# Kernel tuning notes

Hardware: AMD Instinct MI355X
Metric: run time of the kernel (lower is better)

## Reference

```python
import jax, jax.numpy as jnp
import numpy as np

D = 64       # memory_dim
STEPS = 2


def setup_inputs() -> dict:
    key = jax.random.key(0)
    ks = jax.random.split(key, 20)
    N, M, R = 4096, 256, 512
    s = 0.05
    return {
        "coords": jax.random.normal(ks[0], (N, 3), jnp.float32) * 3.0,
        "memory_slots": jax.random.normal(ks[1], (M, D), jnp.float32),
        "anchor_keys": jax.random.normal(ks[2], (M, D), jnp.float32),
        "residue_positions": jax.random.normal(ks[3], (R, 3), jnp.float32) * 3.0,
        "residue_radii": jax.random.uniform(ks[4], (R,), jnp.float32, 0.5, 2.0),
        "W1": jax.random.normal(ks[5], (3, D), jnp.float32) * s,
        "b1": jnp.zeros((D,), jnp.float32),
        "W2": jax.random.normal(ks[6], (D, D), jnp.float32) * s,
        "b2": jnp.zeros((D,), jnp.float32),
        "Wg1": jax.random.normal(ks[7], (2 * D + 2, D), jnp.float32) * s,
        "bg1": jnp.zeros((D,), jnp.float32),
        "Wg2": jax.random.normal(ks[8], (D, 1), jnp.float32) * s,
        "bg2": jnp.zeros((1,), jnp.float32),
        "Wu1": jax.random.normal(ks[9], (2 * D + 2, D), jnp.float32) * s,
        "bu1": jnp.zeros((D,), jnp.float32),
        "Wu2": jax.random.normal(ks[10], (D, D), jnp.float32) * s,
        "bu2": jnp.zeros((D,), jnp.float32),
    }


def _step(points, qe, mem, keys, rpos, rrad,
          Wg1, bg1, Wg2, bg2, Wu1, bu1, Wu2, bu2):
    N = qe.shape[0]
    M = mem.shape[0]
    # attention read
    logits = (qe @ keys.T) / jnp.sqrt(jnp.asarray(D, qe.dtype))     # [N, M]
    rw = jax.nn.softmax(logits, axis=-1)                             # [N, M]
    mc = rw @ mem                                                    # [N, D]
    # SDF gate: cdist(points, residue_positions) -> min over residues
    sq = jnp.sum((points[:, None, :] - rpos[None, :, :]) ** 2, axis=-1)
    geo = jnp.sqrt(jnp.maximum(sq, 0.0))                             # [N, R]
    sdf = jnp.min(geo - rrad[None, :], axis=-1, keepdims=True)       # [N, 1]
    sg = jax.nn.sigmoid(4.0 * sdf)                                   # [N, 1]
    # broadcast-concat -> [N, M, 2D+2]
    write_in = jnp.concatenate([
        jnp.broadcast_to(mc[:, None, :], (N, M, D)),
        jnp.broadcast_to(mem[None, :, :], (N, M, D)),
        rw[:, :, None],
        jnp.broadcast_to(sg[:, None, :], (N, M, 1)),
    ], axis=-1)
    gate = jax.nn.sigmoid(jax.nn.silu(write_in @ Wg1 + bg1) @ Wg2 + bg2)
    gate = jnp.mean(gate, axis=0)                                    # [M, 1]
    delta = jax.nn.silu(write_in @ Wu1 + bu1) @ Wu2 + bu2
    delta = jnp.mean(delta, axis=0)                                  # [M, D]
    mem2 = mem + gate * delta
    return mc, rw, gate, sg, mem2


def reference(coords, memory_slots, anchor_keys, residue_positions, residue_radii,
              W1, b1, W2, b2, Wg1, bg1, Wg2, bg2, Wu1, bu1, Wu2, bu2):
    points = coords.reshape(-1, 3)
    qe = jax.nn.silu(points @ W1 + b1) @ W2 + b2                     # coord_proj
    mem = memory_slots
    for _ in range(max(STEPS, 1)):
        mc, rw, gate, sg, mem = _step(points, qe, mem, anchor_keys,
                                      residue_positions, residue_radii,
                                      Wg1, bg1, Wg2, bg2, Wu1, bu1, Wu2, bu2)
        qe = qe + 0.5 * mc
    # (memory_context, read_weights, write_gate, symbolic_gate, updated_memory)
    return mc, rw, gate[:, 0], sg[:, 0], mem
```

## Files before the change

### kernel.cpp

```cpp
#include <hip/hip_runtime.h>
#include <hip/hip_bf16.h>
#include <math.h>

#define DD 64
#define LOG2E 1.44269504f
#define LN2 0.69314718f
#define NEG_L2E (-1.44269504f)

__device__ __forceinline__ float frcp(float x) { return __builtin_amdgcn_rcpf(x); }
__device__ __forceinline__ float fsig(float x) { return frcp(1.0f + __expf(-x)); }
__device__ __forceinline__ float fsilu(float x) { return x * fsig(x); }
__device__ __forceinline__ float rcp1p(float e) {
  float y = 1.0f + e;
  float r = __uint_as_float(0x7EF127EAu - __float_as_uint(y));
  return r * fmaf(-y, r, 2.0f);
}

__global__ __launch_bounds__(DD) void k_coord(
    const float* __restrict__ coords, const float* __restrict__ W1,
    const float* __restrict__ b1, const float* __restrict__ W2,
    const float* __restrict__ b2, float* __restrict__ qe, int N) {
  int n = blockIdx.x;
  int k = threadIdx.x;
  __shared__ float h[DD];
  float px = coords[n * 3 + 0], py = coords[n * 3 + 1], pz = coords[n * 3 + 2];
  float t = px * W1[k] + py * W1[DD + k] + pz * W1[2 * DD + k] + b1[k];
  h[k] = fsilu(t);
  __syncthreads();
  float q = b2[k];
#pragma unroll 8
  for (int j = 0; j < DD; j++) q += h[j] * W2[j * DD + k];
  qe[n * DD + k] = q;
}

__global__ __launch_bounds__(256) void k_prep(
    const float* __restrict__ keys, float* __restrict__ keysT, int M) {
  int j = blockIdx.x;
  int t = threadIdx.x;
  keysT[j * M + t] = keys[t * DD + j];
}

__global__ __launch_bounds__(DD) void k_scale(
    const float* __restrict__ Wg1, const float* __restrict__ Wu1,
    const float* __restrict__ Wg2, float* __restrict__ wg1r_n,
    float* __restrict__ wu1r_n, float* __restrict__ w2n) {
  int k = threadIdx.x;
  wg1r_n[k] = Wg1[128 * DD + k] * NEG_L2E;
  wu1r_n[k] = Wu1[128 * DD + k] * NEG_L2E;
  w2n[k] = -Wg2[k] * LN2;
}

__global__ __launch_bounds__(256) void k_sdf(
    const float* __restrict__ rpos, const float* __restrict__ rrad,
    const float* __restrict__ coords, float* __restrict__ sg_out, int N, int R) {
  int wv = threadIdx.x >> 6, ln = threadIdx.x & 63;
  int n = blockIdx.x * 4 + wv;
  if (n >= N) return;
  float px = coords[n * 3], py = coords[n * 3 + 1], pz = coords[n * 3 + 2];
  float mn = 1e30f;
  for (int r = ln; r < R; r += 64) {
    float dx = px - rpos[r * 3], dy = py - rpos[r * 3 + 1], dz = pz - rpos[r * 3 + 2];
    float d = sqrtf(dx * dx + dy * dy + dz * dz) - rrad[r];
    mn = fminf(mn, d);
  }
  mn = fminf(mn, __shfl_xor(mn, 32, 64));
  mn = fminf(mn, __shfl_xor(mn, 16, 64));
  mn = fminf(mn, __shfl_xor(mn, 8, 64));
  mn = fminf(mn, __shfl_xor(mn, 4, 64));
  mn = fminf(mn, __shfl_xor(mn, 2, 64));
  mn = fminf(mn, __shfl_xor(mn, 1, 64));
  if (ln == 0) sg_out[n] = fsig(4.0f * mn);
}

__global__ __launch_bounds__(256) void k_attn(
    const float* __restrict__ qe_in, const float* __restrict__ keysT,
    const float* __restrict__ mem, const float* __restrict__ sg,
    const float* __restrict__ Wg1, const float* __restrict__ bg1,
    const float* __restrict__ Wu1, const float* __restrict__ bu1,
    float* __restrict__ rw_out, float* __restrict__ rwT,
    float* __restrict__ mc_out, float* __restrict__ qe_io,
    float* __restrict__ AgT4, float* __restrict__ Au, int N, int M, int NCH2) {
  int bx = blockIdx.x;
  int c = bx % NCH2;
  int j2 = bx / NCH2;
  int n0 = c * 128 + j2 * 4;
  int t = threadIdx.x;
  int wv = t >> 6, ln = t & 63;
  __shared__ __align__(16) float rws[4][256];
  __shared__ __align__(16) float mcs[4][DD];
  __shared__ float red[4][4], red2[4][4];
  __shared__ float part[4][4][DD];
  float lg[4] = {0.f, 0.f, 0.f, 0.f};
#pragma unroll 8
  for (int j = 0; j < DD; j++) {
    float kv = keysT[j * M + t];
    lg[0] += qe_in[(size_t)(n0 + 0) * DD + j] * kv;
    lg[1] += qe_in[(size_t)(n0 + 1) * DD + j] * kv;
    lg[2] += qe_in[(size_t)(n0 + 2) * DD + j] * kv;
    lg[3] += qe_in[(size_t)(n0 + 3) * DD + j] * kv;
  }
  float e[4];
#pragma unroll
  for (int q = 0; q < 4; q++) {
    float x = lg[q] * 0.125f;
    lg[q] = x;
    float mx = x;
    mx = fmaxf(mx, __shfl_xor(mx, 32, 64));
    mx = fmaxf(mx, __shfl_xor(mx, 16, 64));
    mx = fmaxf(mx, __shfl_xor(mx, 8, 64));
    mx = fmaxf(mx, __shfl_xor(mx, 4, 64));
    mx = fmaxf(mx, __shfl_xor(mx, 2, 64));
    mx = fmaxf(mx, __shfl_xor(mx, 1, 64));
    if (ln == 0) red[q][wv] = mx;
  }
  __syncthreads();
#pragma unroll
  for (int q = 0; q < 4; q++) {
    float mx = fmaxf(fmaxf(red[q][0], red[q][1]), fmaxf(red[q][2], red[q][3]));
    float ee = __expf(lg[q] - mx);
    e[q] = ee;
    float sm = ee;
    sm += __shfl_xor(sm, 32, 64);
    sm += __shfl_xor(sm, 16, 64);
    sm += __shfl_xor(sm, 8, 64);
    sm += __shfl_xor(sm, 4, 64);
    sm += __shfl_xor(sm, 2, 64);
    sm += __shfl_xor(sm, 1, 64);
    if (ln == 0) red2[q][wv] = sm;
  }
  __syncthreads();
  float rv4[4];
#pragma unroll
  for (int q = 0; q < 4; q++) {
    float tot = red2[q][0] + red2[q][1] + red2[q][2] + red2[q][3];
    float rv = e[q] * frcp(tot);
    rw_out[(size_t)(n0 + q) * M + t] = rv;
    rws[q][t] = rv;
    rv4[q] = rv;
  }
  *reinterpret_cast<float4*>(&rwT[(size_t)t * N + n0]) =
      make_float4(rv4[0], rv4[1], rv4[2], rv4[3]);
  __syncthreads();
  float acc[4] = {0.f, 0.f, 0.f, 0.f};
#pragma unroll
  for (int mm4 = 0; mm4 < 16; mm4++) {
    int mbase = wv * 64 + mm4 * 4;
    const float4 r0 = *reinterpret_cast<const float4*>(&rws[0][mbase]);
    const float4 r1 = *reinterpret_cast<const float4*>(&rws[1][mbase]);
    const float4 r2 = *reinterpret_cast<const float4*>(&rws[2][mbase]);
    const float4 r3 = *reinterpret_cast<const float4*>(&rws[3][mbase]);
    float m0v = mem[(size_t)(mbase + 0) * DD + ln];
    float m1v = mem[(size_t)(mbase + 1) * DD + ln];
    float m2v = mem[(size_t)(mbase + 2) * DD + ln];
    float m3v = mem[(size_t)(mbase + 3) * DD + ln];
    acc[0] += r0.x * m0v + r0.y * m1v + r0.z * m2v + r0.w * m3v;
    acc[1] += r1.x * m0v + r1.y * m1v + r1.z * m2v + r1.w * m3v;
    acc[2] += r2.x * m0v + r2.y * m1v + r2.z * m2v + r2.w * m3v;
    acc[3] += r3.x * m0v + r3.y * m1v + r3.z * m2v + r3.w * m3v;
  }
#pragma unroll
  for (int q = 0; q < 4; q++) part[q][wv][ln] = acc[q];
  __syncthreads();
  {
    int q = wv;
    float mc = part[q][0][ln] + part[q][1][ln] + part[q][2][ln] + part[q][3][ln];
    mc_out[(size_t)(n0 + q) * DD + ln] = mc;
    qe_io[(size_t)(n0 + q) * DD + ln] =
        qe_in[(size_t)(n0 + q) * DD + ln] + 0.5f * mc;
    mcs[q][ln] = mc;
  }
  __syncthreads();
  {
    const float* W = (wv < 2) ? Wg1 : Wu1;
    const float* bb = (wv < 2) ? bg1 : bu1;
    int qa = (wv & 1) * 2, qb = qa + 1;
    int k = ln;
    float w129 = W[129 * DD + k];
    float bbk = bb[k];
    float a0 = bbk + sg[n0 + qa] * w129;
    float a1 = bbk + sg[n0 + qb] * w129;
#pragma unroll
    for (int j4 = 0; j4 < 16; j4++) {
      const float4 ma = *reinterpret_cast<const float4*>(&mcs[qa][j4 * 4]);
      const float4 mb = *reinterpret_cast<const float4*>(&mcs[qb][j4 * 4]);
      float w0 = W[(size_t)(j4 * 4 + 0) * DD + k];
      float w1 = W[(size_t)(j4 * 4 + 1) * DD + k];
      float w2v = W[(size_t)(j4 * 4 + 2) * DD + k];
      float w3 = W[(size_t)(j4 * 4 + 3) * DD + k];
      a0 += ma.x * w0 + ma.y * w1 + ma.z * w2v + ma.w * w3;
      a1 += mb.x * w0 + mb.y * w1 + mb.z * w2v + mb.w * w3;
    }
    a0 *= NEG_L2E;
    a1 *= NEG_L2E;
    if (wv < 2) {
      AgT4[((size_t)(k >> 2) * N + n0 + qa) * 4 + (k & 3)] = a0;
      AgT4[((size_t)(k >> 2) * N + n0 + qb) * 4 + (k & 3)] = a1;
    } else {
      Au[(size_t)(n0 + qa) * DD + k] = a0;
      Au[(size_t)(n0 + qb) * DD + k] = a1;
    }
  }
}

__global__ __launch_bounds__(128) void k_b(
    const float* __restrict__ mem, const float* __restrict__ Wg1,
    const float* __restrict__ Wu1, float* __restrict__ BgT,
    float* __restrict__ Bu, int M) {
  int m = blockIdx.x;
  int t = threadIdx.x;
  __shared__ float row[DD];
  if (t < DD) row[t] = mem[m * DD + t];
  __syncthreads();
  int k = t & 63;
  const float* W = (t < DD) ? Wg1 : Wu1;
  float b = 0.f;
#pragma unroll 8
  for (int j = 0; j < DD; j++) b += row[j] * W[(DD + j) * DD + k];
  b *= NEG_L2E;
  if (t < DD) BgT[k * M + m] = b;
  else Bu[m * DD + k] = b;
}

__global__ __launch_bounds__(128) void k_write(
    const float* __restrict__ rwT, const float* __restrict__ AgT4,
    const float* __restrict__ Au, const float* __restrict__ BgT,
    const float* __restrict__ Bu, const float* __restrict__ wg1r_n,
    const float* __restrict__ wu1r_n, const float* __restrict__ w2n,
    const float* __restrict__ bg2, float* __restrict__ gate_part,
    float* __restrict__ su_part, int N, int M, int NCH2) {
  int bx = blockIdx.x;
  int c = bx % NCH2;
  int m0 = (bx / NCH2) * 4;
  int wave = threadIdx.x >> 6, lane = threadIdx.x & 63;
  int n0 = __builtin_amdgcn_readfirstlane(c * 128 + wave * 64);

  float rwl[4];
#pragma unroll
  for (int mi = 0; mi < 4; mi++)
    rwl[mi] = rwT[(size_t)(m0 + mi) * N + n0 + lane];
  float gacc[4] = {0.f, 0.f, 0.f, 0.f};
  const float* agp = &AgT4[(size_t)(n0 + lane) * 4];
  float4 ag_cur = *reinterpret_cast<const float4*>(agp);
#pragma unroll
  for (int k4 = 0; k4 < 16; k4++) {
    float4 ag_next = (k4 < 15)
        ? *reinterpret_cast<const float4*>(agp + (size_t)(k4 + 1) * N * 4)
        : ag_cur;
    float agv[4] = {ag_cur.x, ag_cur.y, ag_cur.z, ag_cur.w};
#pragma unroll
    for (int kk = 0; kk < 4; kk++) {
      int k = k4 * 4 + kk;
      const float4 bg4 =
          *reinterpret_cast<const float4*>(&BgT[k * M + m0]);
      float bgv[4] = {bg4.x, bg4.y, bg4.z, bg4.w};
      float wr = wg1r_n[k];
      float w2 = w2n[k];
#pragma unroll
      for (int mi = 0; mi < 4; mi++) {
        float tp = fmaf(rwl[mi], wr, agv[kk] + bgv[mi]);
        float ee = __builtin_amdgcn_exp2f(tp);
        gacc[mi] = fmaf(tp * w2, rcp1p(ee), gacc[mi]);
      }
    }
    ag_cur = ag_next;
  }
  float bg2v = bg2[0];
  float gate[4];
#pragma unroll
  for (int mi = 0; mi < 4; mi++) {
    float g = fsig(gacc[mi] + bg2v);
    g += __shfl_xor(g, 32, 64);
    g += __shfl_xor(g, 16, 64);
    g += __shfl_xor(g, 8, 64);
    g += __shfl_xor(g, 4, 64);
    g += __shfl_xor(g, 2, 64);
    g += __shfl_xor(g, 1, 64);
    gate[mi] = g;
  }

  float bu[4];
#pragma unroll
  for (int mi = 0; mi < 4; mi++) bu[mi] = Bu[(size_t)(m0 + mi) * DD + lane];
  float wu = wu1r_n[lane];
  float su[4] = {0.f, 0.f, 0.f, 0.f};
  const float* Aup = Au + (size_t)n0 * DD + lane;
  const float* r0p = rwT + (size_t)(m0 + 0) * N + n0;
  const float* r1p = rwT + (size_t)(m0 + 1) * N + n0;
  const float* r2p = rwT + (size_t)(m0 + 2) * N + n0;
  const float* r3p = rwT + (size_t)(m0 + 3) * N + n0;
  float au_cur = Aup[0];
#pragma unroll 8
  for (int i = 0; i < 64; i++) {
    float au_next = (i < 63) ? Aup[(size_t)(i + 1) * DD] : au_cur;
    float rvs[4] = {r0p[i], r1p[i], r2p[i], r3p[i]};
#pragma unroll
    for (int mi = 0; mi < 4; mi++) {
      float tp = fmaf(rvs[mi], wu, au_cur + bu[mi]);
      float ee = __builtin_amdgcn_exp2f(tp);
      su[mi] = fmaf(tp, rcp1p(ee), su[mi]);
    }
    au_cur = au_next;
  }

  __shared__ float su_s[2][4][DD];
  __shared__ float g_s[2][4];
#pragma unroll
  for (int mi = 0; mi < 4; mi++) su_s[wave][mi][lane] = su[mi];
  if (lane == 0) {
#pragma unroll
    for (int mi = 0; mi < 4; mi++) g_s[wave][mi] = gate[mi];
  }
  __syncthreads();
  if (threadIdx.x < DD) {
    int k = threadIdx.x;
#pragma unroll
    for (int mi = 0; mi < 4; mi++) {
      su_part[((size_t)(m0 + mi) * NCH2 + c) * DD + k] =
          (su_s[0][mi][k] + su_s[1][mi][k]) * (-LN2);
      if (k == 0)
        gate_part[(m0 + mi) * NCH2 + c] = g_s[0][mi] + g_s[1][mi];
    }
  }
}

__global__ __launch_bounds__(128) void k_reduce_b(
    const float* __restrict__ gate_part, const float* __restrict__ su_part,
    const float* __restrict__ Wu2, const float* __restrict__ bu2,
    const float* __restrict__ mem_in, const float* __restrict__ Wg1,
    const float* __restrict__ Wu1, float* __restrict__ mem_out,
    float* __restrict__ gate_out, float* __restrict__ BgT,
    float* __restrict__ Bu, int N, int M, int NCH2) {
  int m = blockIdx.x;
  int t = threadIdx.x;
  int k = t & 63;
  __shared__ float su_s[DD];
  __shared__ float row[DD];
  __shared__ float gmean;
  float invN = frcp((float)N);
  if (t < DD) {
    float s = 0.f;
    for (int c = 0; c < NCH2; c++) s += su_part[((size_t)m * NCH2 + c) * DD + k];
    su_s[k] = s * invN;
    if (k == 0) {
      float g = 0.f;
      for (int c = 0; c < NCH2; c++) g += gate_part[m * NCH2 + c];
      gmean = g * invN;
    }
  }
  __syncthreads();
  if (t < DD) {
    float delta = bu2[k];
#pragma unroll 8
    for (int j = 0; j < DD; j++) delta += su_s[j] * Wu2[j * DD + k];
    float v = mem_in[m * DD + k] + gmean * delta;
    mem_out[m * DD + k] = v;
    row[k] = v;
    if (k == 0) gate_out[m] = gmean;
  }
  __syncthreads();
  const float* W = (t < DD) ? Wg1 : Wu1;
  float b = 0.f;
#pragma unroll 8
  for (int j = 0; j < DD; j++) b += row[j] * W[(DD + j) * DD + k];
  b *= NEG_L2E;
  if (t < DD) BgT[k * M + m] = b;
  else Bu[m * DD + k] = b;
}

extern "C" void kernel_launch(void* const* d_in, const int* in_sizes, int n_in,
                              void* d_out, int out_size, void* d_ws, size_t ws_size,
                              hipStream_t stream) {
  const float* coords = (const float*)d_in[0];
  const float* memory_slots = (const float*)d_in[1];
  const float* anchor_keys = (const float*)d_in[2];
  const float* rpos = (const float*)d_in[3];
  const float* rrad = (const float*)d_in[4];
  const float* W1 = (const float*)d_in[5];
  const float* b1 = (const float*)d_in[6];
  const float* W2 = (const float*)d_in[7];
  const float* b2 = (const float*)d_in[8];
  const float* Wg1 = (const float*)d_in[9];
  const float* bg1 = (const float*)d_in[10];
  const float* Wg2 = (const float*)d_in[11];
  const float* bg2 = (const float*)d_in[12];
  const float* Wu1 = (const float*)d_in[13];
  const float* bu1 = (const float*)d_in[14];
  const float* Wu2 = (const float*)d_in[15];
  const float* bu2 = (const float*)d_in[16];

  const int N = in_sizes[0] / 3;
  const int M = in_sizes[1] / DD;
  const int R = in_sizes[4];
  const int NCH2 = N / 128;

  float* out = (float*)d_out;
  float* out_mc = out;
  float* out_rw = out_mc + (size_t)N * DD;
  float* out_gate = out_rw + (size_t)N * M;
  float* out_sg = out_gate + M;
  float* out_mem = out_sg + N;

  float* ws = (float*)d_ws;
  float* qe = ws;        ws += (size_t)N * DD;
  float* AgT4 = ws;      ws += (size_t)N * DD;
  float* Au = ws;        ws += (size_t)N * DD;
  float* rwT = ws;       ws += (size_t)M * N;
  float* keysT = ws;     ws += (size_t)DD * M;
  float* BgT = ws;       ws += (size_t)DD * M;
  float* Bu = ws;        ws += (size_t)M * DD;
  float* wg1r_n = ws;    ws += DD;
  float* wu1r_n = ws;    ws += DD;
  float* w2n = ws;       ws += DD;
  float* gate_part = ws; ws += (size_t)M * NCH2;
  float* su_part = ws;   ws += (size_t)M * NCH2 * DD;

  k_coord<<<N, DD, 0, stream>>>(coords, W1, b1, W2, b2, qe, N);
  k_prep<<<DD, M, 0, stream>>>(anchor_keys, keysT, M);
  k_scale<<<1, DD, 0, stream>>>(Wg1, Wu1, Wg2, wg1r_n, wu1r_n, w2n);
  k_sdf<<<N / 4, 256, 0, stream>>>(rpos, rrad, coords, out_sg, N, R);
  k_b<<<M, 128, 0, stream>>>(memory_slots, Wg1, Wu1, BgT, Bu, M);

  const float* mem_cur = memory_slots;
  for (int step = 0; step < 2; step++) {
    k_attn<<<N / 4, 256, 0, stream>>>(qe, keysT, mem_cur, out_sg, Wg1, bg1, Wu1,
                                      bu1, out_rw, rwT, out_mc, qe, AgT4, Au,
                                      N, M, NCH2);
    k_write<<<(M / 4) * NCH2, 128, 0, stream>>>(rwT, AgT4, Au, BgT, Bu,
                                                wg1r_n, wu1r_n, w2n, bg2,
                                                gate_part, su_part, N, M, NCH2);
    k_reduce_b<<<M, 128, 0, stream>>>(gate_part, su_part, Wu2, bu2, mem_cur,
                                      Wg1, Wu1, out_mem, out_gate, BgT, Bu,
                                      N, M, NCH2);
    mem_cur = out_mem;
  }
}
```

Baseline: 144.3 us.

## Fuse setup kernels into one launch and split write kernel into gate/update blocks

Merges the five setup kernels (coord projection, key transpose, weight scaling, SDF gate, B precompute) into one block-indexed k_setup launch to cut launch overhead. It also splits k_write over a second grid dimension so the gate and update reductions run in separate blocks in parallel instead of serially in one block. This doubles k_write's block count and shortens each block's critical path, at the cost of reading rwT twice and running some setup blocks with idle threads.

```diff
diff --git a/kernel.cpp b/kernel.cpp
--- a/kernel.cpp
+++ b/kernel.cpp
@@ -16,60 +16,77 @@
   return r * fmaf(-y, r, 2.0f);
 }
 
-__global__ __launch_bounds__(DD) void k_coord(
+__global__ __launch_bounds__(256) void k_setup(
     const float* __restrict__ coords, const float* __restrict__ W1,
     const float* __restrict__ b1, const float* __restrict__ W2,
-    const float* __restrict__ b2, float* __restrict__ qe, int N) {
-  int n = blockIdx.x;
-  int k = threadIdx.x;
-  __shared__ float h[DD];
-  float px = coords[n * 3 + 0], py = coords[n * 3 + 1], pz = coords[n * 3 + 2];
-  float t = px * W1[k] + py * W1[DD + k] + pz * W1[2 * DD + k] + b1[k];
-  h[k] = fsilu(t);
-  __syncthreads();
-  float q = b2[k];
-#pragma unroll 8
-  for (int j = 0; j < DD; j++) q += h[j] * W2[j * DD + k];
-  qe[n * DD + k] = q;
-}
-
-__global__ __launch_bounds__(256) void k_prep(
-    const float* __restrict__ keys, float* __restrict__ keysT, int M) {
-  int j = blockIdx.x;
-  int t = threadIdx.x;
-  keysT[j * M + t] = keys[t * DD + j];
-}
-
-__global__ __launch_bounds__(DD) void k_scale(
-    const float* __restrict__ Wg1, const float* __restrict__ Wu1,
-    const float* __restrict__ Wg2, float* __restrict__ wg1r_n,
-    float* __restrict__ wu1r_n, float* __restrict__ w2n) {
-  int k = threadIdx.x;
-  wg1r_n[k] = Wg1[128 * DD + k] * NEG_L2E;
-  wu1r_n[k] = Wu1[128 * DD + k] * NEG_L2E;
-  w2n[k] = -Wg2[k] * LN2;
-}
-
-__global__ __launch_bounds__(256) void k_sdf(
+    const float* __restrict__ b2, const float* __restrict__ keys,
     const float* __restrict__ rpos, const float* __restrict__ rrad,
-    const float* __restrict__ coords, float* __restrict__ sg_out, int N, int R) {
-  int wv = threadIdx.x >> 6, ln = threadIdx.x & 63;
-  int n = blockIdx.x * 4 + wv;
-  if (n >= N) return;
-  float px = coords[n * 3], py = coords[n * 3 + 1], pz = coords[n * 3 + 2];
-  float mn = 1e30f;
-  for (int r = ln; r < R; r += 64) {
-    float dx = px - rpos[r * 3], dy = py - rpos[r * 3 + 1], dz = pz - rpos[r * 3 + 2];
-    float d = sqrtf(dx * dx + dy * dy + dz * dz) - rrad[r];
-    mn = fminf(mn, d);
-  }
-  mn = fminf(mn, __shfl_xor(mn, 32, 64));
-  mn = fminf(mn, __shfl_xor(mn, 16, 64));
-  mn = fminf(mn, __shfl_xor(mn, 8, 64));
-  mn = fminf(mn, __shfl_xor(mn, 4, 64));
-  mn = fminf(mn, __shfl_xor(mn, 2, 64));
-  mn = fminf(mn, __shfl_xor(mn, 1, 64));
-  if (ln == 0) sg_out[n] = fsig(4.0f * mn);
+    const float* __restrict__ mem, const float* __restrict__ Wg1,
+    const float* __restrict__ Wu1, const float* __restrict__ Wg2,
+    float* __restrict__ qe, float* __restrict__ keysT,
+    float* __restrict__ sg_out, float* __restrict__ BgT,
+    float* __restrict__ Bu, float* __restrict__ wg1r_n,
+    float* __restrict__ wu1r_n, float* __restrict__ w2n, int N, int M, int R) {
+  int bx = blockIdx.x;
+  int NB4 = N / 4;
+  if (bx < NB4) {
+    int sub = threadIdx.x >> 6, k = threadIdx.x & 63;
+    int n = bx * 4 + sub;
+    __shared__ float h[4][DD];
+    float px = coords[n * 3 + 0], py = coords[n * 3 + 1], pz = coords[n * 3 + 2];
+    float t = px * W1[k] + py * W1[DD + k] + pz * W1[2 * DD + k] + b1[k];
+    h[sub][k] = fsilu(t);
+    __syncthreads();
+    float q = b2[k];
+#pragma unroll 8
+    for (int j = 0; j < DD; j++) q += h[sub][j] * W2[j * DD + k];
+    qe[(size_t)n * DD + k] = q;
+  } else if (bx < 2 * NB4) {
+    int wv = threadIdx.x >> 6, ln = threadIdx.x & 63;
+    int n = (bx - NB4) * 4 + wv;
+    float px = coords[n * 3], py = coords[n * 3 + 1], pz = coords[n * 3 + 2];
+    float mn = 1e30f;
+    for (int r = ln; r < R; r += 64) {
+      float dx = px - rpos[r * 3], dy = py - rpos[r * 3 + 1],
+            dz = pz - rpos[r * 3 + 2];
+      float d = sqrtf(dx * dx + dy * dy + dz * dz) - rrad[r];
+      mn = fminf(mn, d);
+    }
+    mn = fminf(mn, __shfl_xor(mn, 32, 64));
+    mn = fminf(mn, __shfl_xor(mn, 16, 64));
+    mn = fminf(mn, __shfl_xor(mn, 8, 64));
+    mn = fminf(mn, __shfl_xor(mn, 4, 64));
+    mn = fminf(mn, __shfl_xor(mn, 2, 64));
+    mn = fminf(mn, __shfl_xor(mn, 1, 64));
+    if (ln == 0) sg_out[n] = fsig(4.0f * mn);
+  } else if (bx < 2 * NB4 + DD) {
+    int j = bx - 2 * NB4;
+    int t = threadIdx.x;
+    keysT[j * M + t] = keys[t * DD + j];
+  } else if (bx < 2 * NB4 + DD + M) {
+    int m = bx - (2 * NB4 + DD);
+    int t = threadIdx.x;
+    __shared__ float row[DD];
+    if (t < DD) row[t] = mem[m * DD + t];
+    __syncthreads();
+    if (t < 128) {
+      int k = t & 63;
+      const float* W = (t < DD) ? Wg1 : Wu1;
+      float b = 0.f;
+#pragma unroll 8
+      for (int j = 0; j < DD; j++) b += row[j] * W[(DD + j) * DD + k];
+      b *= NEG_L2E;
+      if (t < DD) BgT[k * M + m] = b;
+      else Bu[m * DD + k] = b;
+    }
+  } else {
+    int k = threadIdx.x;
+    if (k < DD) {
+      wg1r_n[k] = Wg1[128 * DD + k] * NEG_L2E;
+      wu1r_n[k] = Wu1[128 * DD + k] * NEG_L2E;
+      w2n[k] = -Wg2[k] * LN2;
+    }
+  }
 }
 
 __global__ __launch_bounds__(256) void k_attn(
@@ -202,25 +219,6 @@
   }
 }
 
-__global__ __launch_bounds__(128) void k_b(
-    const float* __restrict__ mem, const float* __restrict__ Wg1,
-    const float* __restrict__ Wu1, float* __restrict__ BgT,
-    float* __restrict__ Bu, int M) {
-  int m = blockIdx.x;
-  int t = threadIdx.x;
-  __shared__ float row[DD];
-  if (t < DD) row[t] = mem[m * DD + t];
-  __syncthreads();
-  int k = t & 63;
-  const float* W = (t < DD) ? Wg1 : Wu1;
-  float b = 0.f;
-#pragma unroll 8
-  for (int j = 0; j < DD; j++) b += row[j] * W[(DD + j) * DD + k];
-  b *= NEG_L2E;
-  if (t < DD) BgT[k * M + m] = b;
-  else Bu[m * DD + k] = b;
-}
-
 __global__ __launch_bounds__(128) void k_write(
     const float* __restrict__ rwT, const float* __restrict__ AgT4,
     const float* __restrict__ Au, const float* __restrict__ BgT,
@@ -234,91 +232,90 @@
   int wave = threadIdx.x >> 6, lane = threadIdx.x & 63;
   int n0 = __builtin_amdgcn_readfirstlane(c * 128 + wave * 64);
 
-  float rwl[4];
-#pragma unroll
-  for (int mi = 0; mi < 4; mi++)
-    rwl[mi] = rwT[(size_t)(m0 + mi) * N + n0 + lane];
-  float gacc[4] = {0.f, 0.f, 0.f, 0.f};
-  const float* agp = &AgT4[(size_t)(n0 + lane) * 4];
-  float4 ag_cur = *reinterpret_cast<const float4*>(agp);
-#pragma unroll
-  for (int k4 = 0; k4 < 16; k4++) {
-    float4 ag_next = (k4 < 15)
-        ? *reinterpret_cast<const float4*>(agp + (size_t)(k4 + 1) * N * 4)
-        : ag_cur;
-    float agv[4] = {ag_cur.x, ag_cur.y, ag_cur.z, ag_cur.w};
-#pragma unroll
-    for (int kk = 0; kk < 4; kk++) {
-      int k = k4 * 4 + kk;
-      const float4 bg4 =
-          *reinterpret_cast<const float4*>(&BgT[k * M + m0]);
-      float bgv[4] = {bg4.x, bg4.y, bg4.z, bg4.w};
-      float wr = wg1r_n[k];
-      float w2 = w2n[k];
+  if (blockIdx.y == 0) {
+    __shared__ float g_s[2][4];
+    float rwl[4];
+#pragma unroll
+    for (int mi = 0; mi < 4; mi++)
+      rwl[mi] = rwT[(size_t)(m0 + mi) * N + n0 + lane];
+    float gacc[4] = {0.f, 0.f, 0.f, 0.f};
+    const float* agp = &AgT4[(size_t)(n0 + lane) * 4];
+    float4 ag_cur = *reinterpret_cast<const float4*>(agp);
+#pragma unroll
+    for (int k4 = 0; k4 < 16; k4++) {
+      float4 ag_next = (k4 < 15)
+          ? *reinterpret_cast<const float4*>(agp + (size_t)(k4 + 1) * N * 4)
+          : ag_cur;
+      float agv[4] = {ag_cur.x, ag_cur.y, ag_cur.z, ag_cur.w};
+#pragma unroll
+      for (int kk = 0; kk < 4; kk++) {
+        int k = k4 * 4 + kk;
+        const float4 bg4 =
+            *reinterpret_cast<const float4*>(&BgT[k * M + m0]);
+        float bgv[4] = {bg4.x, bg4.y, bg4.z, bg4.w};
+        float wr = wg1r_n[k];
+        float w2 = w2n[k];
+#pragma unroll
+        for (int mi = 0; mi < 4; mi++) {
+          float tp = fmaf(rwl[mi], wr, agv[kk] + bgv[mi]);
+          float ee = __builtin_amdgcn_exp2f(tp);
+          gacc[mi] = fmaf(tp * w2, rcp1p(ee), gacc[mi]);
+        }
+      }
+      ag_cur = ag_next;
+    }
+    float bg2v = bg2[0];
+#pragma unroll
+    for (int mi = 0; mi < 4; mi++) {
+      float g = fsig(gacc[mi] + bg2v);
+      g += __shfl_xor(g, 32, 64);
+      g += __shfl_xor(g, 16, 64);
+      g += __shfl_xor(g, 8, 64);
+      g += __shfl_xor(g, 4, 64);
+      g += __shfl_xor(g, 2, 64);
+      g += __shfl_xor(g, 1, 64);
+      if (lane == 0) g_s[wave][mi] = g;
+    }
+    __syncthreads();
+    if (threadIdx.x < 4) {
+      int mi = threadIdx.x;
+      gate_part[(m0 + mi) * NCH2 + c] = g_s[0][mi] + g_s[1][mi];
+    }
+  } else {
+    __shared__ float su_s[2][4][DD];
+    float bu[4];
+#pragma unroll
+    for (int mi = 0; mi < 4; mi++) bu[mi] = Bu[(size_t)(m0 + mi) * DD + lane];
+    float wu = wu1r_n[lane];
+    float su[4] = {0.f, 0.f, 0.f, 0.f};
+    const float* Aup = Au + (size_t)n0 * DD + lane;
+    const float* r0p = rwT + (size_t)(m0 + 0) * N + n0;
+    const float* r1p = rwT + (size_t)(m0 + 1) * N + n0;
+    const float* r2p = rwT + (size_t)(m0 + 2) * N + n0;
+    const float* r3p = rwT + (size_t)(m0 + 3) * N + n0;
+    float au_cur = Aup[0];
+#pragma unroll 8
+    for (int i = 0; i < 64; i++) {
+      float au_next = (i < 63) ? Aup[(size_t)(i + 1) * DD] : au_cur;
+      float rvs[4] = {r0p[i], r1p[i], r2p[i], r3p[i]};
 #pragma unroll
       for (int mi = 0; mi < 4; mi++) {
-        float tp = fmaf(rwl[mi], wr, agv[kk] + bgv[mi]);
+        float tp = fmaf(rvs[mi], wu, au_cur + bu[mi]);
         float ee = __builtin_amdgcn_exp2f(tp);
-        gacc[mi] = fmaf(tp * w2, rcp1p(ee), gacc[mi]);
+        su[mi] = fmaf(tp, rcp1p(ee), su[mi]);
       }
-    }
-    ag_cur = ag_next;
-  }
-  float bg2v = bg2[0];
-  float gate[4];
-#pragma unroll
-  for (int mi = 0; mi < 4; mi++) {
-    float g = fsig(gacc[mi] + bg2v);
-    g += __shfl_xor(g, 32, 64);
-    g += __shfl_xor(g, 16, 64);
-    g += __shfl_xor(g, 8, 64);
-    g += __shfl_xor(g, 4, 64);
-    g += __shfl_xor(g, 2, 64);
-    g += __shfl_xor(g, 1, 64);
-    gate[mi] = g;
-  }
-
-  float bu[4];
-#pragma unroll
-  for (int mi = 0; mi < 4; mi++) bu[mi] = Bu[(size_t)(m0 + mi) * DD + lane];
-  float wu = wu1r_n[lane];
-  float su[4] = {0.f, 0.f, 0.f, 0.f};
-  const float* Aup = Au + (size_t)n0 * DD + lane;
-  const float* r0p = rwT + (size_t)(m0 + 0) * N + n0;
-  const float* r1p = rwT + (size_t)(m0 + 1) * N + n0;
-  const float* r2p = rwT + (size_t)(m0 + 2) * N + n0;
-  const float* r3p = rwT + (size_t)(m0 + 3) * N + n0;
-  float au_cur = Aup[0];
-#pragma unroll 8
-  for (int i = 0; i < 64; i++) {
-    float au_next = (i < 63) ? Aup[(size_t)(i + 1) * DD] : au_cur;
-    float rvs[4] = {r0p[i], r1p[i], r2p[i], r3p[i]};
-#pragma unroll
-    for (int mi = 0; mi < 4; mi++) {
-      float tp = fmaf(rvs[mi], wu, au_cur + bu[mi]);
-      float ee = __builtin_amdgcn_exp2f(tp);
-      su[mi] = fmaf(tp, rcp1p(ee), su[mi]);
-    }
-    au_cur = au_next;
-  }
-
-  __shared__ float su_s[2][4][DD];
-  __shared__ float g_s[2][4];
-#pragma unroll
-  for (int mi = 0; mi < 4; mi++) su_s[wave][mi][lane] = su[mi];
-  if (lane == 0) {
-#pragma unroll
-    for (int mi = 0; mi < 4; mi++) g_s[wave][mi] = gate[mi];
-  }
-  __syncthreads();
-  if (threadIdx.x < DD) {
-    int k = threadIdx.x;
-#pragma unroll
-    for (int mi = 0; mi < 4; mi++) {
-      su_part[((size_t)(m0 + mi) * NCH2 + c) * DD + k] =
-          (su_s[0][mi][k] + su_s[1][mi][k]) * (-LN2);
-      if (k == 0)
-        gate_part[(m0 + mi) * NCH2 + c] = g_s[0][mi] + g_s[1][mi];
+      au_cur = au_next;
+    }
+#pragma unroll
+    for (int mi = 0; mi < 4; mi++) su_s[wave][mi][lane] = su[mi];
+    __syncthreads();
+    if (threadIdx.x < DD) {
+      int k = threadIdx.x;
+#pragma unroll
+      for (int mi = 0; mi < 4; mi++) {
+        su_part[((size_t)(m0 + mi) * NCH2 + c) * DD + k] =
+            (su_s[0][mi][k] + su_s[1][mi][k]) * (-LN2);
+      }
     }
   }
 }
@@ -414,20 +411,19 @@
   float* gate_part = ws; ws += (size_t)M * NCH2;
   float* su_part = ws;   ws += (size_t)M * NCH2 * DD;
 
-  k_coord<<<N, DD, 0, stream>>>(coords, W1, b1, W2, b2, qe, N);
-  k_prep<<<DD, M, 0, stream>>>(anchor_keys, keysT, M);
-  k_scale<<<1, DD, 0, stream>>>(Wg1, Wu1, Wg2, wg1r_n, wu1r_n, w2n);
-  k_sdf<<<N / 4, 256, 0, stream>>>(rpos, rrad, coords, out_sg, N, R);
-  k_b<<<M, 128, 0, stream>>>(memory_slots, Wg1, Wu1, BgT, Bu, M);
+  int setup_blocks = (N / 4) * 2 + DD + M + 1;
+  k_setup<<<setup_blocks, 256, 0, stream>>>(
+      coords, W1, b1, W2, b2, anchor_keys, rpos, rrad, memory_slots, Wg1, Wu1,
+      Wg2, qe, keysT, out_sg, BgT, Bu, wg1r_n, wu1r_n, w2n, N, M, R);
 
   const float* mem_cur = memory_slots;
   for (int step = 0; step < 2; step++) {
     k_attn<<<N / 4, 256, 0, stream>>>(qe, keysT, mem_cur, out_sg, Wg1, bg1, Wu1,
                                       bu1, out_rw, rwT, out_mc, qe, AgT4, Au,
                                       N, M, NCH2);
-    k_write<<<(M / 4) * NCH2, 128, 0, stream>>>(rwT, AgT4, Au, BgT, Bu,
-                                                wg1r_n, wu1r_n, w2n, bg2,
-                                                gate_part, su_part, N, M, NCH2);
+    k_write<<<dim3((M / 4) * NCH2, 2), 128, 0, stream>>>(
+        rwT, AgT4, Au, BgT, Bu, wg1r_n, wu1r_n, w2n, bg2, gate_part, su_part,
+        N, M, NCH2);
     k_reduce_b<<<M, 128, 0, stream>>>(gate_part, su_part, Wu2, bu2, mem_cur,
                                       Wg1, Wu1, out_mem, out_gate, BgT, Bu,
                                       N, M, NCH2);
```

Result: slower. 158.8 us (+10.1%).
